# Kernel optimization log

Measured on AMD Instinct MI355X. Metric: run time of the kernel, lower is better.

Reference implementation:

```python
import jax, jax.numpy as jnp
import numpy as np

FEATHER = (16, 16)          # in_feather_size
OUT_FEATHER = (16, 16)      # out_feather_size
F = FEATHER[0] * FEATHER[1]            # 256
INNER = (F + 1) ** 2                   # 66049
OUT = OUT_FEATHER[0] * OUT_FEATHER[1]  # 256
B = 2048


def setup_inputs() -> dict:
    key = jax.random.key(0)
    kx, kw, kb = jax.random.split(key, 3)
    x = jax.random.normal(kx, (B, F), dtype=jnp.float32)
    # nn.Linear(INNER, OUT): weight [OUT, INNER], bias [OUT]
    bound = 1.0 / np.sqrt(INNER)
    W = jax.random.uniform(kw, (OUT, INNER), dtype=jnp.float32, minval=-bound, maxval=bound)
    b = jax.random.uniform(kb, (OUT,), dtype=jnp.float32, minval=-bound, maxval=bound)
    return {"x": x, "W": W, "b": b}


def reference(x, W, b):
    # x: [B, F] -> prepend 1 -> x1: [B, F+1]
    x = x.reshape(-1, F)
    ones = jnp.ones((x.shape[0], 1), dtype=x.dtype)
    x1 = jnp.concatenate([ones, x], axis=-1)          # [B, F+1]
    # batched outer product, flattened: [B, (F+1)^2]
    outer = (x1[:, :, None] * x1[:, None, :]).reshape(x.shape[0], INNER)
    y = outer @ W.T + b                               # [B, OUT]
    return y.reshape(-1, OUT_FEATHER[0], OUT_FEATHER[1])
```

## Files before the change

### kernel.cpp

```cpp
#include <hip/hip_runtime.h>
#include <cstdint>
#include <cstddef>


typedef _Float16 half8 __attribute__((ext_vector_type(8)));
typedef float    f32x4 __attribute__((ext_vector_type(4)));

#define KSPLIT 16

#define WAITVM(N) asm volatile("s_waitcnt vmcnt(" #N ")" ::: "memory")
#define WAITLGKM  asm volatile("s_waitcnt lgkmcnt(0)" ::: "memory")

__device__ __forceinline__ void gload_lds16(const void* g, void* lds) {
  __builtin_amdgcn_global_load_lds(
      (const __attribute__((address_space(1))) uint32_t*)g,
      (__attribute__((address_space(3))) uint32_t*)lds, 16, 0, 0);
}

__global__ void conv_w_k(const float* __restrict__ W, _Float16* __restrict__ Wp) {
  int t   = blockIdx.x * 256 + threadIdx.x;
  int j8  = t & 31;
  int rem = t >> 5;
  int ii  = rem % 258;
  int o   = rem / 258;
  float v[8];
  if (ii < 257) {
    const float* src = W + (size_t)o * 66049 + ii * 257 + j8 * 8;
#pragma unroll
    for (int u = 0; u < 8; ++u) v[u] = src[u];
  } else {
    const float* src = W + (size_t)o * 66049 + 256;
#pragma unroll
    for (int u = 0; u < 8; ++u) v[u] = src[(size_t)(j8 * 8 + u) * 257];
  }
  half8 h;
#pragma unroll
  for (int u = 0; u < 8; ++u) h[u] = (_Float16)v[u];
  *(half8*)(Wp + ((size_t)o * 258 + ii) * 256 + j8 * 8) = h;
}

__global__ void conv_x1_k(const float* __restrict__ x, _Float16* __restrict__ X1g) {
  int t  = blockIdx.x * 256 + threadIdx.x;
  int j8 = t % 33;
  int b  = t / 33;
  half8 h;
#pragma unroll
  for (int u = 0; u < 8; ++u) {
    int jj = j8 * 8 + u;
    float v = (jj == 0) ? 1.0f : (jj <= 256 ? x[(size_t)b * 256 + (jj - 1)] : 0.0f);
    h[u] = (_Float16)v;
  }
  *(half8*)(X1g + (size_t)b * 264 + j8 * 8) = h;
}

__global__ void init_out_k(const float* __restrict__ x, const float* __restrict__ W,
                           const float* __restrict__ bias, float* __restrict__ Y) {
  int o = threadIdx.x;
  int b = blockIdx.x;
  float xl = x[(size_t)b * 256 + 255];
  float w  = W[(size_t)o * 66049 + 66048];
  Y[(size_t)b * 256 + o] = bias[o] + xl * xl * w;
}

__global__ __launch_bounds__(512, 2)
void gemm_k(const _Float16* __restrict__ Wp, const _Float16* __restrict__ X1g,
            float* __restrict__ Y) {
  __shared__ __align__(16) _Float16 wbuf[4 * 8192];
  __shared__ _Float16 scal[17 * 128];

  const int bid = blockIdx.x;
  const int s   = bid & (KSPLIT - 1);
  const int mt  = bid >> 4;
  const int nii = 16 + (s < 2 ? 1 : 0);
  const int ii0 = s * 16 + (s < 2 ? s : 2);

  const int tid = threadIdx.x;
  const int l   = tid & 63;
  const int w   = tid >> 6;
  const int wm  = w >> 2;
  const int wn  = w & 3;
  const int ln  = l & 15;
  const int ks  = l >> 4;

  for (int t = tid; t < nii * 128; t += 512) {
    int k = t >> 7, m = t & 127;
    int ii = ii0 + k; if (ii > 256) ii = 256;
    scal[k * 128 + m] = X1g[(size_t)(mt * 128 + m) * 264 + ii];
  }

  half8 base[4][8];
  {
    const _Float16* xr = X1g + (size_t)(mt * 128 + wm * 64 + ln) * 264 + ks * 8;
#pragma unroll
    for (int mf = 0; mf < 4; ++mf)
#pragma unroll
      for (int jc = 0; jc < 8; ++jc)
        base[mf][jc] = *(const half8*)(xr + (size_t)mf * (16 * 264) + jc * 32);
  }

  f32x4 acc[4][4];
#pragma unroll
  for (int mf = 0; mf < 4; ++mf)
#pragma unroll
    for (int nf = 0; nf < 4; ++nf) acc[mf][nf] = (f32x4){0.f, 0.f, 0.f, 0.f};

  auto stage = [&](int buf, int ii, int jc) {
#pragma unroll
    for (int t2 = 0; t2 < 2; ++t2) {
      int f = t2 * 8 + w;
      const _Float16* g = Wp + ((size_t)(f * 16 + ln) * 258 + ii) * 256 + jc * 32 + ks * 8;
      gload_lds16(g, (char*)wbuf + buf * 16384 + f * 1024);
    }
  };

  const int nsteps = nii * 8;
  stage(0, ii0, 0);
  stage(1, ii0, 1);
  stage(2, ii0, 2);
  WAITVM(4);
  WAITLGKM;
  __builtin_amdgcn_s_barrier();

  for (int iio = 0; iio < nii; ++iio) {
    half8 s8[4];
#pragma unroll
    for (int mf = 0; mf < 4; ++mf) {
      _Float16 sv = scal[iio * 128 + wm * 64 + mf * 16 + ln];
      s8[mf] = (half8){sv, sv, sv, sv, sv, sv, sv, sv};
    }
#pragma unroll
    for (int jc = 0; jc < 8; ++jc) {
      const int st  = iio * 8 + jc;
      const int st3 = st + 3;
      if (st3 < nsteps) stage(st3 & 3, ii0 + (st3 >> 3), st3 & 7);

      half8 af[4];
#pragma unroll
      for (int mf = 0; mf < 4; ++mf) af[mf] = base[mf][jc] * s8[mf];

      const _Float16* wb = wbuf + (st & 3) * 8192 + (wn * 4) * 512 + l * 8;
#pragma unroll
      for (int nf = 0; nf < 4; ++nf) {
        half8 bf = *(const half8*)(wb + nf * 512);
#pragma unroll
        for (int mf = 0; mf < 4; ++mf)
          acc[mf][nf] = __builtin_amdgcn_mfma_f32_16x16x32_f16(af[mf], bf, acc[mf][nf], 0, 0, 0);
      }
      const int rem = nsteps - 1 - st;
      if (rem >= 3)      { WAITVM(4); }
      else if (rem == 2) { WAITVM(2); }
      else if (rem == 1) { WAITVM(0); }
      WAITLGKM;
      __builtin_amdgcn_s_barrier();
    }
  }

  float* yb = Y + (size_t)(mt * 128 + wm * 64) * 256 + wn * 64;
  const int r0 = ks * 4;
#pragma unroll
  for (int mf = 0; mf < 4; ++mf)
#pragma unroll
    for (int nf = 0; nf < 4; ++nf)
#pragma unroll
      for (int r = 0; r < 4; ++r)
        unsafeAtomicAdd(&yb[(size_t)(mf * 16 + r0 + r) * 256 + nf * 16 + ln],
                        acc[mf][nf][r]);
}

__global__ void fb_k(const float* __restrict__ x, const float* __restrict__ W,
                     const float* __restrict__ bias, float* __restrict__ Y) {
  __shared__ float x1[257];
  int b = blockIdx.x, o = threadIdx.x;
  x1[o + 1] = x[(size_t)b * 256 + o];
  if (o == 0) x1[0] = 1.0f;
  __syncthreads();
  const float* Wr = W + (size_t)o * 66049;
  float acc = bias[o];
  for (int i = 0; i < 257; ++i) {
    const float* wr = Wr + (size_t)i * 257;
    float p = 0.f;
    for (int j = 0; j < 257; ++j) p = fmaf(x1[j], wr[j], p);
    acc = fmaf(x1[i], p, acc);
  }
  Y[(size_t)b * 256 + o] = acc;
}

extern "C" void kernel_launch(void* const* d_in, const int* in_sizes, int n_in,
                              void* d_out, int out_size, void* d_ws, size_t ws_size,
                              hipStream_t stream) {
  const float* x = (const float*)d_in[0];
  const float* W = (const float*)d_in[1];
  const float* b = (const float*)d_in[2];
  float* y = (float*)d_out;

  const size_t WPB = (size_t)256 * 258 * 256 * 2;
  const size_t X1B = (size_t)2048 * 264 * 2;
  if (ws_size < WPB + X1B) {
    fb_k<<<2048, 256, 0, stream>>>(x, W, b, y);
    return;
  }
  _Float16* Wp  = (_Float16*)d_ws;
  _Float16* X1g = (_Float16*)((char*)d_ws + WPB);

  conv_w_k<<<8256, 256, 0, stream>>>(W, Wp);
  conv_x1_k<<<264, 256, 0, stream>>>(x, X1g);
  init_out_k<<<2048, 256, 0, stream>>>(x, W, b, y);
  gemm_k<<<256, 512, 0, stream>>>(Wp, X1g, y);
}
```

Measured before the change: 142.9 us.

## Load W fragments directly into registers with double buffering instead of LDS staging

Replaces the LDS ring buffer for W tiles, filled with global_load_lds, by per-wave direct global loads into registers with a two-deep register double buffer. This removes the per-step barriers and the LDS write/read round trip, and raises wave priority around the MFMA blocks. In exchange, waves that share the same W columns each fetch them separately, which increases global/L2 traffic. The prefetch lookahead also shrinks, which may expose memory latency.

After: 164.8 us. 1.15x slower.

```diff
diff --git a/kernel.cpp b/kernel.cpp
--- a/kernel.cpp
+++ b/kernel.cpp
@@ -7,15 +7,6 @@
 typedef float    f32x4 __attribute__((ext_vector_type(4)));
 
 #define KSPLIT 16
-
-#define WAITVM(N) asm volatile("s_waitcnt vmcnt(" #N ")" ::: "memory")
-#define WAITLGKM  asm volatile("s_waitcnt lgkmcnt(0)" ::: "memory")
-
-__device__ __forceinline__ void gload_lds16(const void* g, void* lds) {
-  __builtin_amdgcn_global_load_lds(
-      (const __attribute__((address_space(1))) uint32_t*)g,
-      (__attribute__((address_space(3))) uint32_t*)lds, 16, 0, 0);
-}
 
 __global__ void conv_w_k(const float* __restrict__ W, _Float16* __restrict__ Wp) {
   int t   = blockIdx.x * 256 + threadIdx.x;
@@ -65,7 +56,6 @@
 __global__ __launch_bounds__(512, 2)
 void gemm_k(const _Float16* __restrict__ Wp, const _Float16* __restrict__ X1g,
             float* __restrict__ Y) {
-  __shared__ __align__(16) _Float16 wbuf[4 * 8192];
   __shared__ _Float16 scal[17 * 128];
 
   const int bid = blockIdx.x;
@@ -104,56 +94,57 @@
 #pragma unroll
     for (int nf = 0; nf < 4; ++nf) acc[mf][nf] = (f32x4){0.f, 0.f, 0.f, 0.f};
 
-  auto stage = [&](int buf, int ii, int jc) {
-#pragma unroll
-    for (int t2 = 0; t2 < 2; ++t2) {
-      int f = t2 * 8 + w;
-      const _Float16* g = Wp + ((size_t)(f * 16 + ln) * 258 + ii) * 256 + jc * 32 + ks * 8;
-      gload_lds16(g, (char*)wbuf + buf * 16384 + f * 1024);
-    }
-  };
-
-  const int nsteps = nii * 8;
-  stage(0, ii0, 0);
-  stage(1, ii0, 1);
-  stage(2, ii0, 2);
-  WAITVM(4);
-  WAITLGKM;
-  __builtin_amdgcn_s_barrier();
+  const _Float16* wq0 = Wp + (size_t)((wn * 4 + 0) * 16 + ln) * 66048 + ii0 * 256 + ks * 8;
+  const _Float16* wq1 = Wp + (size_t)((wn * 4 + 1) * 16 + ln) * 66048 + ii0 * 256 + ks * 8;
+  const _Float16* wq2 = Wp + (size_t)((wn * 4 + 2) * 16 + ln) * 66048 + ii0 * 256 + ks * 8;
+  const _Float16* wq3 = Wp + (size_t)((wn * 4 + 3) * 16 + ln) * 66048 + ii0 * 256 + ks * 8;
+
+#define LOADW(dst, st)                                         \
+  do {                                                         \
+    dst[0] = *(const half8*)(wq0 + (size_t)(st) * 32);         \
+    dst[1] = *(const half8*)(wq1 + (size_t)(st) * 32);         \
+    dst[2] = *(const half8*)(wq2 + (size_t)(st) * 32);         \
+    dst[3] = *(const half8*)(wq3 + (size_t)(st) * 32);         \
+  } while (0)
+
+  half8 wA[4], wB[4];
+  LOADW(wA, 0);
+
+  __syncthreads();
 
   for (int iio = 0; iio < nii; ++iio) {
-    half8 s8[4];
+    half8 sv8[4];
 #pragma unroll
     for (int mf = 0; mf < 4; ++mf) {
       _Float16 sv = scal[iio * 128 + wm * 64 + mf * 16 + ln];
-      s8[mf] = (half8){sv, sv, sv, sv, sv, sv, sv, sv};
+      sv8[mf] = (half8){sv, sv, sv, sv, sv, sv, sv, sv};
     }
 #pragma unroll
-    for (int jc = 0; jc < 8; ++jc) {
-      const int st  = iio * 8 + jc;
-      const int st3 = st + 3;
-      if (st3 < nsteps) stage(st3 & 3, ii0 + (st3 >> 3), st3 & 7);
-
-      half8 af[4];
-#pragma unroll
-      for (int mf = 0; mf < 4; ++mf) af[mf] = base[mf][jc] * s8[mf];
-
-      const _Float16* wb = wbuf + (st & 3) * 8192 + (wn * 4) * 512 + l * 8;
-#pragma unroll
-      for (int nf = 0; nf < 4; ++nf) {
-        half8 bf = *(const half8*)(wb + nf * 512);
-#pragma unroll
-        for (int mf = 0; mf < 4; ++mf)
-          acc[mf][nf] = __builtin_amdgcn_mfma_f32_16x16x32_f16(af[mf], bf, acc[mf][nf], 0, 0, 0);
+    for (int jcp = 0; jcp < 8; jcp += 2) {
+      const int st = iio * 8 + jcp;
+      LOADW(wB, st + 1);
+      __builtin_amdgcn_s_setprio(1);
+#pragma unroll
+      for (int mf = 0; mf < 4; ++mf) {
+        half8 af = base[mf][jcp] * sv8[mf];
+#pragma unroll
+        for (int nf = 0; nf < 4; ++nf)
+          acc[mf][nf] = __builtin_amdgcn_mfma_f32_16x16x32_f16(af, wA[nf], acc[mf][nf], 0, 0, 0);
       }
-      const int rem = nsteps - 1 - st;
-      if (rem >= 3)      { WAITVM(4); }
-      else if (rem == 2) { WAITVM(2); }
-      else if (rem == 1) { WAITVM(0); }
-      WAITLGKM;
-      __builtin_amdgcn_s_barrier();
+      __builtin_amdgcn_s_setprio(0);
+      LOADW(wA, st + 2);
+      __builtin_amdgcn_s_setprio(1);
+#pragma unroll
+      for (int mf = 0; mf < 4; ++mf) {
+        half8 af = base[mf][jcp + 1] * sv8[mf];
+#pragma unroll
+        for (int nf = 0; nf < 4; ++nf)
+          acc[mf][nf] = __builtin_amdgcn_mfma_f32_16x16x32_f16(af, wB[nf], acc[mf][nf], 0, 0, 0);
+      }
+      __builtin_amdgcn_s_setprio(0);
     }
   }
+#undef LOADW
 
   float* yb = Y + (size_t)(mt * 128 + wm * 64) * 256 + wn * 64;
   const int r0 = ks * 4;
```

## Pre-tile fp16 weights in MFMA order and double K-split with jc-outer loop

Applied to the files above, without the earlier changes.

The weight conversion kernel now writes W into a layout that is already tiled in MFMA fragment order, so each gemm stage is two contiguous 16-byte global-to-LDS loads per lane. The gemm now splits K 32 ways instead of 16 and launches 512 blocks, with launch bounds raised to 4 blocks per CU. The loop order is swapped so the x1 fragment for each jc is loaded once and reused across the ii values, replacing a large register-resident base array. MFMA sections are wrapped in s_setprio, and the final barrier is skipped. The cost is twice as many atomic adds into Y and a more complex staging index.

After: 145.9 us. 1.02x slower.

```diff
diff --git a/kernel.cpp b/kernel.cpp
--- a/kernel.cpp
+++ b/kernel.cpp
@@ -6,8 +6,7 @@
 typedef _Float16 half8 __attribute__((ext_vector_type(8)));
 typedef float    f32x4 __attribute__((ext_vector_type(4)));
 
-#define KSPLIT 16
-
+#define LD8(p) (*(const half8*)(p))
 #define WAITVM(N) asm volatile("s_waitcnt vmcnt(" #N ")" ::: "memory")
 #define WAITLGKM  asm volatile("s_waitcnt lgkmcnt(0)" ::: "memory")
 
@@ -18,25 +17,24 @@
 }
 
 __global__ void conv_w_k(const float* __restrict__ W, _Float16* __restrict__ Wp) {
-  int t   = blockIdx.x * 256 + threadIdx.x;
-  int j8  = t & 31;
-  int rem = t >> 5;
-  int ii  = rem % 258;
-  int o   = rem / 258;
-  float v[8];
+  int t  = blockIdx.x * 256 + threadIdx.x;
+  int l  = t & 63;
+  int f  = (t >> 6) & 15;
+  int jc = (t >> 10) & 7;
+  int ii = t >> 13;
+  int o  = f * 16 + (l & 15);
+  int j0 = jc * 32 + (l >> 4) * 8;
+  half8 h;
   if (ii < 257) {
-    const float* src = W + (size_t)o * 66049 + ii * 257 + j8 * 8;
-#pragma unroll
-    for (int u = 0; u < 8; ++u) v[u] = src[u];
+    const float* src = W + (size_t)o * 66049 + (size_t)ii * 257 + j0;
+#pragma unroll
+    for (int e = 0; e < 8; ++e) h[e] = (_Float16)src[e];
   } else {
     const float* src = W + (size_t)o * 66049 + 256;
 #pragma unroll
-    for (int u = 0; u < 8; ++u) v[u] = src[(size_t)(j8 * 8 + u) * 257];
-  }
-  half8 h;
-#pragma unroll
-  for (int u = 0; u < 8; ++u) h[u] = (_Float16)v[u];
-  *(half8*)(Wp + ((size_t)o * 258 + ii) * 256 + j8 * 8) = h;
+    for (int e = 0; e < 8; ++e) h[e] = (_Float16)src[(size_t)(j0 + e) * 257];
+  }
+  *(half8*)(Wp + (size_t)t * 8) = h;
 }
 
 __global__ void conv_x1_k(const float* __restrict__ x, _Float16* __restrict__ X1g) {
@@ -62,17 +60,17 @@
   Y[(size_t)b * 256 + o] = bias[o] + xl * xl * w;
 }
 
-__global__ __launch_bounds__(512, 2)
+__global__ __launch_bounds__(512, 4)
 void gemm_k(const _Float16* __restrict__ Wp, const _Float16* __restrict__ X1g,
             float* __restrict__ Y) {
   __shared__ __align__(16) _Float16 wbuf[4 * 8192];
-  __shared__ _Float16 scal[17 * 128];
+  __shared__ _Float16 scal[9 * 128];
 
   const int bid = blockIdx.x;
-  const int s   = bid & (KSPLIT - 1);
-  const int mt  = bid >> 4;
-  const int nii = 16 + (s < 2 ? 1 : 0);
-  const int ii0 = s * 16 + (s < 2 ? s : 2);
+  const int s   = bid & 31;
+  const int mt  = bid >> 5;
+  const int nii = (s < 2) ? 9 : 8;
+  const int ii0 = s * 8 + (s < 2 ? s : 2);
 
   const int tid = threadIdx.x;
   const int l   = tid & 63;
@@ -88,70 +86,95 @@
     scal[k * 128 + m] = X1g[(size_t)(mt * 128 + m) * 264 + ii];
   }
 
-  half8 base[4][8];
-  {
-    const _Float16* xr = X1g + (size_t)(mt * 128 + wm * 64 + ln) * 264 + ks * 8;
-#pragma unroll
-    for (int mf = 0; mf < 4; ++mf)
-#pragma unroll
-      for (int jc = 0; jc < 8; ++jc)
-        base[mf][jc] = *(const half8*)(xr + (size_t)mf * (16 * 264) + jc * 32);
-  }
-
-  f32x4 acc[4][4];
-#pragma unroll
-  for (int mf = 0; mf < 4; ++mf)
-#pragma unroll
-    for (int nf = 0; nf < 4; ++nf) acc[mf][nf] = (f32x4){0.f, 0.f, 0.f, 0.f};
-
-  auto stage = [&](int buf, int ii, int jc) {
-#pragma unroll
-    for (int t2 = 0; t2 < 2; ++t2) {
-      int f = t2 * 8 + w;
-      const _Float16* g = Wp + ((size_t)(f * 16 + ln) * 258 + ii) * 256 + jc * 32 + ks * 8;
-      gload_lds16(g, (char*)wbuf + buf * 16384 + f * 1024);
-    }
-  };
+  const _Float16* xr = X1g + (size_t)(mt * 128 + wm * 64 + ln) * 264 + ks * 8;
+
+  const char* gW   = (const char*)Wp + (size_t)ii0 * 131072 + w * 1024 + l * 16;
+  char*       ldsW = (char*)wbuf + w * 1024;
 
   const int nsteps = nii * 8;
-  stage(0, ii0, 0);
-  stage(1, ii0, 1);
-  stage(2, ii0, 2);
+
+  gload_lds16(gW +     0, ldsW);            gload_lds16(gW +  8192, ldsW + 8192);
+  gload_lds16(gW + 131072, ldsW + 16384);   gload_lds16(gW + 139264, ldsW + 24576);
+  gload_lds16(gW + 262144, ldsW + 32768);   gload_lds16(gW + 270336, ldsW + 40960);
   WAITVM(4);
   WAITLGKM;
   __builtin_amdgcn_s_barrier();
 
-  for (int iio = 0; iio < nii; ++iio) {
-    half8 s8[4];
-#pragma unroll
-    for (int mf = 0; mf < 4; ++mf) {
-      _Float16 sv = scal[iio * 128 + wm * 64 + mf * 16 + ln];
-      s8[mf] = (half8){sv, sv, sv, sv, sv, sv, sv, sv};
-    }
-#pragma unroll
-    for (int jc = 0; jc < 8; ++jc) {
-      const int st  = iio * 8 + jc;
-      const int st3 = st + 3;
-      if (st3 < nsteps) stage(st3 & 3, ii0 + (st3 >> 3), st3 & 7);
-
-      half8 af[4];
-#pragma unroll
-      for (int mf = 0; mf < 4; ++mf) af[mf] = base[mf][jc] * s8[mf];
+  f32x4 acc[4][4];
+#pragma unroll
+  for (int mf = 0; mf < 4; ++mf)
+#pragma unroll
+    for (int nf = 0; nf < 4; ++nf) acc[mf][nf] = (f32x4){0.f, 0.f, 0.f, 0.f};
+
+  int st  = 0;
+  int sk  = 3, sjc = 0;
+  for (int jc = 0; jc < 8; ++jc) {
+    half8 cur[4];
+#pragma unroll
+    for (int mf = 0; mf < 4; ++mf)
+      cur[mf] = LD8(xr + (size_t)(mf * 16) * 264 + jc * 32);
+
+    for (int k = 0; k < nii; ++k, ++st) {
+      if (st + 3 < nsteps) {
+        const int blk = (sk * 8 + sjc) * 16384;
+        char* d = ldsW + ((st + 3) & 3) * 16384;
+        gload_lds16(gW + blk, d);
+        gload_lds16(gW + blk + 8192, d + 8192);
+        ++sk; if (sk == nii) { sk = 0; ++sjc; }
+      }
+
+      _Float16 sv0 = scal[k * 128 + wm * 64 +  0 + ln];
+      _Float16 sv1 = scal[k * 128 + wm * 64 + 16 + ln];
+      _Float16 sv2 = scal[k * 128 + wm * 64 + 32 + ln];
+      _Float16 sv3 = scal[k * 128 + wm * 64 + 48 + ln];
 
       const _Float16* wb = wbuf + (st & 3) * 8192 + (wn * 4) * 512 + l * 8;
-#pragma unroll
-      for (int nf = 0; nf < 4; ++nf) {
-        half8 bf = *(const half8*)(wb + nf * 512);
-#pragma unroll
-        for (int mf = 0; mf < 4; ++mf)
-          acc[mf][nf] = __builtin_amdgcn_mfma_f32_16x16x32_f16(af[mf], bf, acc[mf][nf], 0, 0, 0);
-      }
-      const int rem = nsteps - 1 - st;
-      if (rem >= 3)      { WAITVM(4); }
-      else if (rem == 2) { WAITVM(2); }
-      else if (rem == 1) { WAITVM(0); }
-      WAITLGKM;
-      __builtin_amdgcn_s_barrier();
+      half8 bf0 = LD8(wb);
+      half8 bf1 = LD8(wb + 512);
+      half8 bf2 = LD8(wb + 1024);
+      half8 bf3 = LD8(wb + 1536);
+
+      __builtin_amdgcn_s_setprio(1);
+      {
+        half8 v0 = {sv0, sv0, sv0, sv0, sv0, sv0, sv0, sv0};
+        half8 af = cur[0] * v0;
+        acc[0][0] = __builtin_amdgcn_mfma_f32_16x16x32_f16(af, bf0, acc[0][0], 0, 0, 0);
+        acc[0][1] = __builtin_amdgcn_mfma_f32_16x16x32_f16(af, bf1, acc[0][1], 0, 0, 0);
+        acc[0][2] = __builtin_amdgcn_mfma_f32_16x16x32_f16(af, bf2, acc[0][2], 0, 0, 0);
+        acc[0][3] = __builtin_amdgcn_mfma_f32_16x16x32_f16(af, bf3, acc[0][3], 0, 0, 0);
+      }
+      {
+        half8 v1 = {sv1, sv1, sv1, sv1, sv1, sv1, sv1, sv1};
+        half8 af = cur[1] * v1;
+        acc[1][0] = __builtin_amdgcn_mfma_f32_16x16x32_f16(af, bf0, acc[1][0], 0, 0, 0);
+        acc[1][1] = __builtin_amdgcn_mfma_f32_16x16x32_f16(af, bf1, acc[1][1], 0, 0, 0);
+        acc[1][2] = __builtin_amdgcn_mfma_f32_16x16x32_f16(af, bf2, acc[1][2], 0, 0, 0);
+        acc[1][3] = __builtin_amdgcn_mfma_f32_16x16x32_f16(af, bf3, acc[1][3], 0, 0, 0);
+      }
+      {
+        half8 v2 = {sv2, sv2, sv2, sv2, sv2, sv2, sv2, sv2};
+        half8 af = cur[2] * v2;
+        acc[2][0] = __builtin_amdgcn_mfma_f32_16x16x32_f16(af, bf0, acc[2][0], 0, 0, 0);
+        acc[2][1] = __builtin_amdgcn_mfma_f32_16x16x32_f16(af, bf1, acc[2][1], 0, 0, 0);
+        acc[2][2] = __builtin_amdgcn_mfma_f32_16x16x32_f16(af, bf2, acc[2][2], 0, 0, 0);
+        acc[2][3] = __builtin_amdgcn_mfma_f32_16x16x32_f16(af, bf3, acc[2][3], 0, 0, 0);
+      }
+      {
+        half8 v3 = {sv3, sv3, sv3, sv3, sv3, sv3, sv3, sv3};
+        half8 af = cur[3] * v3;
+        acc[3][0] = __builtin_amdgcn_mfma_f32_16x16x32_f16(af, bf0, acc[3][0], 0, 0, 0);
+        acc[3][1] = __builtin_amdgcn_mfma_f32_16x16x32_f16(af, bf1, acc[3][1], 0, 0, 0);
+        acc[3][2] = __builtin_amdgcn_mfma_f32_16x16x32_f16(af, bf2, acc[3][2], 0, 0, 0);
+        acc[3][3] = __builtin_amdgcn_mfma_f32_16x16x32_f16(af, bf3, acc[3][3], 0, 0, 0);
+      }
+      __builtin_amdgcn_s_setprio(0);
+
+      if (st < nsteps - 1) {
+        if (st <= nsteps - 4)      { WAITVM(4); }
+        else if (st == nsteps - 3) { WAITVM(2); }
+        else                       { WAITVM(0); }
+        __builtin_amdgcn_s_barrier();
+      }
     }
   }
 
@@ -193,7 +216,7 @@
   const float* b = (const float*)d_in[2];
   float* y = (float*)d_out;
 
-  const size_t WPB = (size_t)256 * 258 * 256 * 2;
+  const size_t WPB = (size_t)258 * 8 * 16 * 64 * 16;
   const size_t X1B = (size_t)2048 * 264 * 2;
   if (ws_size < WPB + X1B) {
     fb_k<<<2048, 256, 0, stream>>>(x, W, b, y);
@@ -205,5 +228,5 @@
   conv_w_k<<<8256, 256, 0, stream>>>(W, Wp);
   conv_x1_k<<<264, 256, 0, stream>>>(x, X1g);
   init_out_k<<<2048, 256, 0, stream>>>(x, W, b, y);
-  gemm_k<<<256, 512, 0, stream>>>(Wp, X1g, y);
-}
+  gemm_k<<<512, 512, 0, stream>>>(Wp, X1g, y);
+}
```
